# Performance work log

Measured on AMD Instinct MI355X. Metric: run time of the kernel, lower is better.

Reference implementation:

```python
import jax, jax.numpy as jnp
import numpy as np

D_IN = 1024
D_OUT = 1024
NUM_HEADS = 16
HEAD_DIM = D_OUT // NUM_HEADS

def setup_inputs() -> dict:
    key = jax.random.key(0)
    ks = jax.random.split(key, 6)
    b, t = 2, 2048
    s = 0.02
    return {
        "x": jax.random.normal(ks[0], (b, t, D_IN), dtype=jnp.float32),
        "Wq": jax.random.normal(ks[1], (D_IN, D_OUT), dtype=jnp.float32) * s,
        "Wk": jax.random.normal(ks[2], (D_IN, D_OUT), dtype=jnp.float32) * s,
        "Wv": jax.random.normal(ks[3], (D_IN, D_OUT), dtype=jnp.float32) * s,
        "Wo": jax.random.normal(ks[4], (D_OUT, D_OUT), dtype=jnp.float32) * s,
        "bo": jax.random.normal(ks[5], (D_OUT,), dtype=jnp.float32) * s,
    }

def reference(x, Wq, Wk, Wv, Wo, bo):
    b, t, _ = x.shape
    # QKV projections -> [b, h, t, d]
    def split_heads(y):
        return y.reshape(b, t, NUM_HEADS, HEAD_DIM).transpose(0, 2, 1, 3)
    q = split_heads(x @ Wq)
    k = split_heads(x @ Wk)
    v = split_heads(x @ Wv)
    # scores [b, h, t, t], causal mask, softmax over keys
    scores = jnp.einsum('bhqd,bhkd->bhqk', q, k)
    causal = jnp.tril(jnp.ones((t, t), dtype=bool))  # True where allowed
    scores = jnp.where(causal, scores, -jnp.inf)
    attn = jax.nn.softmax(scores / jnp.sqrt(jnp.float32(HEAD_DIM)), axis=-1)
    ctx = jnp.einsum('bhqk,bhkd->bhqd', attn, v)
    ctx = ctx.transpose(0, 2, 1, 3).reshape(b, t, D_OUT)
    return ctx @ Wo + bo
```

## Files before the change

### kernel.cpp

```cpp
#include <hip/hip_runtime.h>
#include <hip/hip_bf16.h>
#include <cstdint>
#include <cstddef>


typedef __bf16 bf16_t;
typedef __bf16 bf16x2 __attribute__((ext_vector_type(2)));
typedef __bf16 bf16x4 __attribute__((ext_vector_type(4)));
typedef __bf16 bf16x8 __attribute__((ext_vector_type(8)));
typedef float  f32x4  __attribute__((ext_vector_type(4)));

#define B_SZ 2
#define T_SZ 2048
#define DIN  1024
#define NH   16
#define HD   64

#define SCL_Q (0.125f * 1.44269504088896f)

__device__ __forceinline__ void gld_lds16(const void* g, void* l) {
    __builtin_amdgcn_global_load_lds(
        (const __attribute__((address_space(1))) void*)g,
        (__attribute__((address_space(3))) void*)l,
        16, 0, 0);
}

__global__ __launch_bounds__(256) void prep_kernel(const float* __restrict__ x,
                                                   bf16_t* __restrict__ x_bf,
                                                   const float* __restrict__ Wq,
                                                   const float* __restrict__ Wk,
                                                   const float* __restrict__ Wv,
                                                   const float* __restrict__ Wo,
                                                   bf16_t* __restrict__ Wqkv_t,
                                                   bf16_t* __restrict__ Wo_t) {
    __shared__ float tile[32][33];
    const int bid = blockIdx.x;
    const int tid = threadIdx.x;
    if (bid < 2048) {
        size_t base = ((size_t)bid * 256 + tid) * 8;
        float4 a = *(const float4*)(x + base);
        float4 b = *(const float4*)(x + base + 4);
        bf16x8 v;
        v[0] = (bf16_t)a.x; v[1] = (bf16_t)a.y; v[2] = (bf16_t)a.z; v[3] = (bf16_t)a.w;
        v[4] = (bf16_t)b.x; v[5] = (bf16_t)b.y; v[6] = (bf16_t)b.z; v[7] = (bf16_t)b.w;
        *(bf16x8*)(x_bf + base) = v;
        return;
    }
    const int tb = bid - 2048;
    const int w  = tb >> 10;
    const int t2 = tb & 1023;
    const int c0 = (t2 & 31) * 32, r0 = (t2 >> 5) * 32;
    const float* src = (w == 0) ? Wq : (w == 1) ? Wk : (w == 2) ? Wv : Wo;
    bf16_t* dst = (w < 3) ? (Wqkv_t + (size_t)w * 1024 * 1024) : Wo_t;
    const int tx = tid & 31, ty = tid >> 5;
#pragma unroll
    for (int i = 0; i < 32; i += 8)
        tile[ty + i][tx] = src[(size_t)(r0 + ty + i) * 1024 + c0 + tx];
    __syncthreads();
#pragma unroll
    for (int i = 0; i < 32; i += 8)
        dst[(size_t)(c0 + ty + i) * 1024 + r0 + tx] = (bf16_t)tile[tx][ty + i];
}

__device__ __forceinline__ void gemm_tile_body(const bf16_t* __restrict__ A,
                                               const bf16_t* __restrict__ Bt,
                                               int m0, int n0, int K,
                                               f32x4 acc[4][4],
                                               bf16_t* As, bf16_t* Bs) {
    const int tid  = threadIdx.x;
    const int lane = tid & 63;
    const int wave = tid >> 6;
    const int wr   = (wave >> 1) * 64;
    const int wc   = (wave & 1) * 64;

#pragma unroll
    for (int mi = 0; mi < 4; ++mi)
#pragma unroll
        for (int ni = 0; ni < 4; ++ni)
            acc[mi][ni] = (f32x4){0.f, 0.f, 0.f, 0.f};

    for (int k0 = 0; k0 < K; k0 += 32) {
#pragma unroll
        for (int c = 0; c < 2; ++c) {
            int fb = (wave * 2 + c) * 1024;
            int e  = (fb >> 1) + lane * 8;
            int r  = e >> 5;
            int kk = e & 31;
            gld_lds16(A  + (size_t)(m0 + r) * K + k0 + kk, (char*)As + fb);
            gld_lds16(Bt + (size_t)(n0 + r) * K + k0 + kk, (char*)Bs + fb);
        }
        __syncthreads();

        bf16x8 af[4], bfr[4];
#pragma unroll
        for (int mi = 0; mi < 4; ++mi)
            af[mi] = *(const bf16x8*)(As + (wr + mi * 16 + (lane & 15)) * 32 + ((lane >> 4) * 8));
#pragma unroll
        for (int ni = 0; ni < 4; ++ni)
            bfr[ni] = *(const bf16x8*)(Bs + (wc + ni * 16 + (lane & 15)) * 32 + ((lane >> 4) * 8));
#pragma unroll
        for (int mi = 0; mi < 4; ++mi)
#pragma unroll
            for (int ni = 0; ni < 4; ++ni)
                acc[mi][ni] = __builtin_amdgcn_mfma_f32_16x16x32_bf16(af[mi], bfr[ni], acc[mi][ni], 0, 0, 0);
        __syncthreads();
    }
}

__global__ __launch_bounds__(256, 2) void gemm_qkv_kernel(const bf16_t* __restrict__ A,
                                                          const bf16_t* __restrict__ Bt,
                                                          bf16_t* __restrict__ Qb,
                                                          bf16_t* __restrict__ Kb,
                                                          bf16_t* __restrict__ Vt) {
    __shared__ alignas(16) bf16_t As[128 * 32];
    __shared__ alignas(16) bf16_t Bs[128 * 32];
    const int nTn = 3072 / 128;
    const int bid = (blockIdx.x & 7) * 96 + (blockIdx.x >> 3);
    int m0 = (bid / nTn) * 128;
    int n0 = (bid % nTn) * 128;
    f32x4 acc[4][4];
    gemm_tile_body(A, Bt, m0, n0, DIN, acc, As, Bs);

    const int lane = threadIdx.x & 63;
    const int wave = threadIdx.x >> 6;
    const int wr = (wave >> 1) * 64, wc = (wave & 1) * 64;
#pragma unroll
    for (int mi = 0; mi < 4; ++mi)
#pragma unroll
        for (int ni = 0; ni < 4; ++ni) {
            int t0 = m0 + wr + mi * 16 + ((lane >> 4) * 4);
            int n  = n0 + wc + ni * 16 + (lane & 15);
            int b  = t0 >> 11, tl = t0 & 2047;
            int part = n >> 10, c = n & 1023;
            int h = c >> 6, d = c & 63;
            if (part == 2) {
                bf16x4 pv;
#pragma unroll
                for (int j = 0; j < 4; ++j) pv[j] = (bf16_t)acc[mi][ni][j];
                *(bf16x4*)&Vt[((size_t)(b * NH + h) * HD + d) * T_SZ + tl] = pv;
            } else if (part == 0) {
#pragma unroll
                for (int j = 0; j < 4; ++j)
                    Qb[(((size_t)(b * NH + h) * T_SZ + tl + j) << 6) + d] =
                        (bf16_t)(acc[mi][ni][j] * SCL_Q);
            } else {
#pragma unroll
                for (int j = 0; j < 4; ++j)
                    Kb[(((size_t)(b * NH + h) * T_SZ + tl + j) << 6) + d] =
                        (bf16_t)acc[mi][ni][j];
            }
        }
}

__global__ __launch_bounds__(256, 3) void attn_kernel(const bf16_t* __restrict__ Qb,
                                                      const bf16_t* __restrict__ Kb,
                                                      const bf16_t* __restrict__ Vt,
                                                      bf16_t* __restrict__ ctx) {
    __shared__ alignas(16) bf16_t Ks[2][64 * 64];
    __shared__ alignas(16) bf16_t Vs[2][64 * 64];
    __shared__ alignas(16) bf16_t P_lds[4][16][72];

    const int raw = blockIdx.x;
    const int xcd = raw & 7;
    const int jj  = raw >> 3;
    const int bh  = xcd * 4 + (jj & 3);
    const int qt  = 31 - (jj >> 2);

    const int lane = threadIdx.x & 63;
    const int wave = threadIdx.x >> 6;

    const bf16_t* Qp = Qb + (size_t)bh * T_SZ * HD;
    const bf16_t* Kp = Kb + (size_t)bh * T_SZ * HD;
    const bf16_t* Vp = Vt + (size_t)bh * HD * T_SZ;

    const int q0 = qt * 64 + wave * 16;
    const int rgrp = lane >> 4;
    const int rcol = lane & 15;

    const int st_r  = (lane >> 3);
    const int st_sl = lane & 7;

    bf16x8 qa[2];
#pragma unroll
    for (int s = 0; s < 2; ++s)
        qa[s] = *(const bf16x8*)(Qp + (size_t)(q0 + rcol) * HD + s * 32 + rgrp * 8);

    f32x4 o[4];
#pragma unroll
    for (int di = 0; di < 4; ++di) o[di] = (f32x4){0.f, 0.f, 0.f, 0.f};
    float mrun = -__builtin_inff();
    float lrun = 0.f;

#define STAGE(BUF, KT)                                                          \
    {                                                                           \
        const int k0s = (KT) * 64;                                              \
        _Pragma("unroll")                                                       \
        for (int c = 0; c < 2; ++c) {                                           \
            int r0 = (wave * 2 + c) * 8;                                        \
            int r  = r0 + st_r;                                                 \
            int sl = st_sl ^ (r & 7);                                           \
            gld_lds16(Kp + (size_t)(k0s + r) * HD + sl * 8,                     \
                      (char*)&Ks[BUF][0] + r0 * 128);                           \
            gld_lds16(Vp + (size_t)r * T_SZ + k0s + sl * 8,                     \
                      (char*)&Vs[BUF][0] + r0 * 128);                           \
        }                                                                       \
    }

    STAGE(0, 0);
    __syncthreads();
    int buf = 0;

    for (int kt = 0; kt <= qt; ++kt) {
        if (kt < qt) STAGE(buf ^ 1, kt + 1);

        const char* Kb_l = (const char*)&Ks[buf][0];
        const char* Vb_l = (const char*)&Vs[buf][0];

        f32x4 s_acc[4];
#pragma unroll
        for (int ni = 0; ni < 4; ++ni) s_acc[ni] = (f32x4){0.f, 0.f, 0.f, 0.f};
#pragma unroll
        for (int s = 0; s < 2; ++s)
#pragma unroll
            for (int ni = 0; ni < 4; ++ni) {
                int fr = ni * 16 + rcol;
                bf16x8 kb = *(const bf16x8*)(Kb_l + fr * 128 + (((s * 4 + rgrp) ^ (fr & 7)) << 4));
                s_acc[ni] = __builtin_amdgcn_mfma_f32_16x16x32_bf16(kb, qa[s], s_acc[ni], 0, 0, 0);
            }

        bf16x8 vf[2][4];
#pragma unroll
        for (int s = 0; s < 2; ++s)
#pragma unroll
            for (int di = 0; di < 4; ++di) {
                int fv = di * 16 + rcol;
                vf[s][di] = *(const bf16x8*)(Vb_l + fv * 128 + (((s * 4 + rgrp) ^ (fv & 7)) << 4));
            }

        float ptile[4][4];
        float pmax = -__builtin_inff();
        if (kt == qt) {
            const int qabs = q0 + rcol;
#pragma unroll
            for (int ni = 0; ni < 4; ++ni)
#pragma unroll
                for (int j = 0; j < 4; ++j) {
                    int kidx = qt * 64 + ni * 16 + rgrp * 4 + j;
                    float v = s_acc[ni][j];
                    if (kidx > qabs) v = -__builtin_inff();
                    ptile[ni][j] = v;
                    pmax = fmaxf(pmax, v);
                }
        } else {
#pragma unroll
            for (int ni = 0; ni < 4; ++ni)
#pragma unroll
                for (int j = 0; j < 4; ++j) {
                    float v = s_acc[ni][j];
                    ptile[ni][j] = v;
                    pmax = fmaxf(pmax, v);
                }
        }
        pmax = fmaxf(pmax, __shfl_xor(pmax, 16));
        pmax = fmaxf(pmax, __shfl_xor(pmax, 32));

        const bool fullb = __any(pmax > mrun + 8.f);
        float a_self = 1.f;
        if (fullb) {
            float newm = fmaxf(mrun, pmax);
            a_self = exp2f(mrun - newm);
            mrun = newm;
        }
        float rsum = 0.f;
#pragma unroll
        for (int ni = 0; ni < 4; ++ni)
#pragma unroll
            for (int j = 0; j < 4; ++j) {
                float p = exp2f(ptile[ni][j] - mrun);
                ptile[ni][j] = p;
                rsum += p;
            }
        rsum += __shfl_xor(rsum, 16);
        rsum += __shfl_xor(rsum, 32);
        if (fullb) {
            lrun = lrun * a_self + rsum;
#pragma unroll
            for (int j = 0; j < 4; ++j) {
                float aj = __shfl(a_self, (lane & 48) | (rgrp * 4 + j));
#pragma unroll
                for (int di = 0; di < 4; ++di) o[di][j] *= aj;
            }
        } else {
            lrun += rsum;
        }

#pragma unroll
        for (int ni = 0; ni < 4; ++ni)
#pragma unroll
            for (int jp = 0; jp < 2; ++jp) {
                bf16x2 pk;
                pk[0] = (bf16_t)ptile[ni][2 * jp];
                pk[1] = (bf16_t)ptile[ni][2 * jp + 1];
                *(bf16x2*)&P_lds[wave][rcol][ni * 16 + rgrp * 4 + 2 * jp] = pk;
            }
#pragma unroll
        for (int s = 0; s < 2; ++s) {
            bf16x8 pa = *(const bf16x8*)(&P_lds[wave][rcol][s * 32 + rgrp * 8]);
#pragma unroll
            for (int di = 0; di < 4; ++di)
                o[di] = __builtin_amdgcn_mfma_f32_16x16x32_bf16(pa, vf[s][di], o[di], 0, 0, 0);
        }
        __syncthreads();
        buf ^= 1;
    }
#undef STAGE

    const int b = bh >> 4, h = bh & 15;
    float invl[4];
#pragma unroll
    for (int j = 0; j < 4; ++j) {
        float lj = __shfl(lrun, (lane & 48) | (rgrp * 4 + j));
        invl[j] = 1.f / lj;
    }
#pragma unroll
    for (int di = 0; di < 4; ++di)
#pragma unroll
        for (int j = 0; j < 4; ++j) {
            int q = q0 + rgrp * 4 + j;
            int d = di * 16 + rcol;
            ctx[((size_t)(b * T_SZ + q) * NH + h) * HD + d] = (bf16_t)(o[di][j] * invl[j]);
        }
}

__global__ __launch_bounds__(256, 3) void gemm_out_kernel(const bf16_t* __restrict__ A,
                                                          const bf16_t* __restrict__ Bt,
                                                          const float* __restrict__ bias,
                                                          float* __restrict__ out) {
    __shared__ alignas(16) bf16_t As[64 * 32];
    __shared__ alignas(16) bf16_t Bs[128 * 32];
    const int nTn = 1024 / 128;
    const int bid = (blockIdx.x & 7) * 64 + (blockIdx.x >> 3);
    int m0 = (bid / nTn) * 64;
    int n0 = (bid % nTn) * 128;

    const int tid  = threadIdx.x;
    const int lane = tid & 63;
    const int wave = tid >> 6;
    const int wr   = (wave >> 1) * 32;
    const int wc   = (wave & 1) * 64;

    f32x4 acc[2][4];
#pragma unroll
    for (int mi = 0; mi < 2; ++mi)
#pragma unroll
        for (int ni = 0; ni < 4; ++ni)
            acc[mi][ni] = (f32x4){0.f, 0.f, 0.f, 0.f};

    for (int k0 = 0; k0 < DIN; k0 += 32) {
        {
            int fb = wave * 1024;
            int e  = (fb >> 1) + lane * 8;
            int r  = e >> 5;
            int kk = e & 31;
            gld_lds16(A + (size_t)(m0 + r) * DIN + k0 + kk, (char*)As + fb);
        }
#pragma unroll
        for (int c = 0; c < 2; ++c) {
            int fb = (wave * 2 + c) * 1024;
            int e  = (fb >> 1) + lane * 8;
            int r  = e >> 5;
            int kk = e & 31;
            gld_lds16(Bt + (size_t)(n0 + r) * DIN + k0 + kk, (char*)Bs + fb);
        }
        __syncthreads();

        bf16x8 af[2], bfr[4];
#pragma unroll
        for (int mi = 0; mi < 2; ++mi)
            af[mi] = *(const bf16x8*)(As + (wr + mi * 16 + (lane & 15)) * 32 + ((lane >> 4) * 8));
#pragma unroll
        for (int ni = 0; ni < 4; ++ni)
            bfr[ni] = *(const bf16x8*)(Bs + (wc + ni * 16 + (lane & 15)) * 32 + ((lane >> 4) * 8));
#pragma unroll
        for (int mi = 0; mi < 2; ++mi)
#pragma unroll
            for (int ni = 0; ni < 4; ++ni)
                acc[mi][ni] = __builtin_amdgcn_mfma_f32_16x16x32_bf16(af[mi], bfr[ni], acc[mi][ni], 0, 0, 0);
        __syncthreads();
    }

#pragma unroll
    for (int mi = 0; mi < 2; ++mi)
#pragma unroll
        for (int ni = 0; ni < 4; ++ni) {
            int n = n0 + wc + ni * 16 + (lane & 15);
            float bv = bias[n];
#pragma unroll
            for (int j = 0; j < 4; ++j) {
                int m = m0 + wr + mi * 16 + ((lane >> 4) * 4) + j;
                out[(size_t)m * 1024 + n] = acc[mi][ni][j] + bv;
            }
        }
}

extern "C" void kernel_launch(void* const* d_in, const int* in_sizes, int n_in,
                              void* d_out, int out_size, void* d_ws, size_t ws_size,
                              hipStream_t stream) {
    const float* x  = (const float*)d_in[0];
    const float* Wq = (const float*)d_in[1];
    const float* Wk = (const float*)d_in[2];
    const float* Wv = (const float*)d_in[3];
    const float* Wo = (const float*)d_in[4];
    const float* bo = (const float*)d_in[5];
    float* out = (float*)d_out;

    char* ws = (char*)d_ws;
    bf16_t* x_bf   = (bf16_t*)(ws);
    bf16_t* Wqkv_t = (bf16_t*)(ws + ((size_t)8 << 20));
    bf16_t* Wo_t   = (bf16_t*)(ws + ((size_t)14 << 20));
    bf16_t* Qb     = (bf16_t*)(ws + ((size_t)16 << 20));
    bf16_t* Kb     = (bf16_t*)(ws + ((size_t)24 << 20));
    bf16_t* Vt     = (bf16_t*)(ws + ((size_t)32 << 20));
    bf16_t* ctx    = (bf16_t*)(ws + ((size_t)40 << 20));

    prep_kernel<<<6144, 256, 0, stream>>>(x, x_bf, Wq, Wk, Wv, Wo, Wqkv_t, Wo_t);
    gemm_qkv_kernel<<<32 * 24, 256, 0, stream>>>(x_bf, Wqkv_t, Qb, Kb, Vt);
    attn_kernel<<<B_SZ * NH * 32, 256, 0, stream>>>(Qb, Kb, Vt, ctx);
    gemm_out_kernel<<<64 * 8, 256, 0, stream>>>(ctx, Wo_t, bo, out);
}
```

Before: 174.9 us.

## Widen attention blocks to 128 query rows with 8 waves sharing K/V tiles

The attention kernel now uses 512-thread blocks, so eight waves cover a 128-row query tile and share each staged 64-key K/V tile, halving the number of blocks and the K/V global-to-LDS traffic per query row. The causal mask check becomes per-wave, based on key offset versus the wave's query start. The cross-lane max reduction now runs only when a rescale is needed, and the row-sum reduction moves out of the loop to the epilogue. The cost is bigger blocks with more LDS per block, and waves in the lower half of a tile doing fully masked work on the last key tile, which can hurt occupancy and load balance.

```diff
diff --git a/kernel.cpp b/kernel.cpp
--- a/kernel.cpp
+++ b/kernel.cpp
@@ -152,19 +152,19 @@
         }
 }
 
-__global__ __launch_bounds__(256, 3) void attn_kernel(const bf16_t* __restrict__ Qb,
+__global__ __launch_bounds__(512, 4) void attn_kernel(const bf16_t* __restrict__ Qb,
                                                       const bf16_t* __restrict__ Kb,
                                                       const bf16_t* __restrict__ Vt,
                                                       bf16_t* __restrict__ ctx) {
     __shared__ alignas(16) bf16_t Ks[2][64 * 64];
     __shared__ alignas(16) bf16_t Vs[2][64 * 64];
-    __shared__ alignas(16) bf16_t P_lds[4][16][72];
+    __shared__ alignas(16) bf16_t P_lds[8][16][72];
 
     const int raw = blockIdx.x;
     const int xcd = raw & 7;
     const int jj  = raw >> 3;
     const int bh  = xcd * 4 + (jj & 3);
-    const int qt  = 31 - (jj >> 2);
+    const int qt  = 15 - (jj >> 2);
 
     const int lane = threadIdx.x & 63;
     const int wave = threadIdx.x >> 6;
@@ -173,7 +173,7 @@
     const bf16_t* Kp = Kb + (size_t)bh * T_SZ * HD;
     const bf16_t* Vp = Vt + (size_t)bh * HD * T_SZ;
 
-    const int q0 = qt * 64 + wave * 16;
+    const int q0 = qt * 128 + wave * 16;
     const int rgrp = lane >> 4;
     const int rcol = lane & 15;
 
@@ -191,30 +191,29 @@
     float mrun = -__builtin_inff();
     float lrun = 0.f;
 
+    const int nkt = 2 * qt + 2;
+
 #define STAGE(BUF, KT)                                                          \
     {                                                                           \
         const int k0s = (KT) * 64;                                              \
-        _Pragma("unroll")                                                       \
-        for (int c = 0; c < 2; ++c) {                                           \
-            int r0 = (wave * 2 + c) * 8;                                        \
-            int r  = r0 + st_r;                                                 \
-            int sl = st_sl ^ (r & 7);                                           \
-            gld_lds16(Kp + (size_t)(k0s + r) * HD + sl * 8,                     \
-                      (char*)&Ks[BUF][0] + r0 * 128);                           \
-            gld_lds16(Vp + (size_t)r * T_SZ + k0s + sl * 8,                     \
-                      (char*)&Vs[BUF][0] + r0 * 128);                           \
-        }                                                                       \
+        int r  = wave * 8 + st_r;                                               \
+        int sl = st_sl ^ (r & 7);                                               \
+        gld_lds16(Kp + (size_t)(k0s + r) * HD + sl * 8,                         \
+                  (char*)&Ks[BUF][0] + wave * 1024);                            \
+        gld_lds16(Vp + (size_t)r * T_SZ + k0s + sl * 8,                         \
+                  (char*)&Vs[BUF][0] + wave * 1024);                            \
     }
 
     STAGE(0, 0);
     __syncthreads();
     int buf = 0;
 
-    for (int kt = 0; kt <= qt; ++kt) {
-        if (kt < qt) STAGE(buf ^ 1, kt + 1);
+    for (int kt = 0; kt < nkt; ++kt) {
+        if (kt + 1 < nkt) STAGE(buf ^ 1, kt + 1);
 
         const char* Kb_l = (const char*)&Ks[buf][0];
         const char* Vb_l = (const char*)&Vs[buf][0];
+        const int k0 = kt * 64;
 
         f32x4 s_acc[4];
 #pragma unroll
@@ -239,13 +238,13 @@
 
         float ptile[4][4];
         float pmax = -__builtin_inff();
-        if (kt == qt) {
+        if (k0 + 63 > q0) {
             const int qabs = q0 + rcol;
 #pragma unroll
             for (int ni = 0; ni < 4; ++ni)
 #pragma unroll
                 for (int j = 0; j < 4; ++j) {
-                    int kidx = qt * 64 + ni * 16 + rgrp * 4 + j;
+                    int kidx = k0 + ni * 16 + rgrp * 4 + j;
                     float v = s_acc[ni][j];
                     if (kidx > qabs) v = -__builtin_inff();
                     ptile[ni][j] = v;
@@ -261,15 +260,21 @@
                     pmax = fmaxf(pmax, v);
                 }
         }
-        pmax = fmaxf(pmax, __shfl_xor(pmax, 16));
-        pmax = fmaxf(pmax, __shfl_xor(pmax, 32));
 
         const bool fullb = __any(pmax > mrun + 8.f);
-        float a_self = 1.f;
         if (fullb) {
+            pmax = fmaxf(pmax, __shfl_xor(pmax, 16));
+            pmax = fmaxf(pmax, __shfl_xor(pmax, 32));
             float newm = fmaxf(mrun, pmax);
-            a_self = exp2f(mrun - newm);
+            float a_self = exp2f(mrun - newm);
             mrun = newm;
+            lrun *= a_self;
+#pragma unroll
+            for (int j = 0; j < 4; ++j) {
+                float aj = __shfl(a_self, (lane & 48) | (rgrp * 4 + j));
+#pragma unroll
+                for (int di = 0; di < 4; ++di) o[di][j] *= aj;
+            }
         }
         float rsum = 0.f;
 #pragma unroll
@@ -280,19 +285,7 @@
                 ptile[ni][j] = p;
                 rsum += p;
             }
-        rsum += __shfl_xor(rsum, 16);
-        rsum += __shfl_xor(rsum, 32);
-        if (fullb) {
-            lrun = lrun * a_self + rsum;
-#pragma unroll
-            for (int j = 0; j < 4; ++j) {
-                float aj = __shfl(a_self, (lane & 48) | (rgrp * 4 + j));
-#pragma unroll
-                for (int di = 0; di < 4; ++di) o[di][j] *= aj;
-            }
-        } else {
-            lrun += rsum;
-        }
+        lrun += rsum;
 
 #pragma unroll
         for (int ni = 0; ni < 4; ++ni)
@@ -315,6 +308,8 @@
     }
 #undef STAGE
 
+    lrun += __shfl_xor(lrun, 16);
+    lrun += __shfl_xor(lrun, 32);
     const int b = bh >> 4, h = bh & 15;
     float invl[4];
 #pragma unroll
@@ -425,6 +420,6 @@
 
     prep_kernel<<<6144, 256, 0, stream>>>(x, x_bf, Wq, Wk, Wv, Wo, Wqkv_t, Wo_t);
     gemm_qkv_kernel<<<32 * 24, 256, 0, stream>>>(x_bf, Wqkv_t, Qb, Kb, Vt);
-    attn_kernel<<<B_SZ * NH * 32, 256, 0, stream>>>(Qb, Kb, Vt, ctx);
+    attn_kernel<<<B_SZ * NH * 16, 512, 0, stream>>>(Qb, Kb, Vt, ctx);
     gemm_out_kernel<<<64 * 8, 256, 0, stream>>>(ctx, Wo_t, bo, out);
 }
```

Measured after the change: 182.8 us. +4.5%, slower.
